# Performance work log

Measured on AMD Instinct MI355X. Metric: run time of the kernel, lower is better.

## Reference

```python
import jax, jax.numpy as jnp
import numpy as np

B, T, H, W = 4, 1024, 27, 48
LOOKUP = 101          # must be odd
OUT_DIM = 128
NBINS = 512           # 8 levels per RGB channel -> 8^3


def setup_inputs() -> dict:
    key = jax.random.key(0)
    k1, k2 = jax.random.split(key, 2)
    frames = jax.random.randint(k1, (B, T, H, W, 3), 0, 256, dtype=jnp.int32)
    # nn.Linear(lookup_window, output_dim): weight [out,in] in torch; store transposed [in,out]
    bound = 1.0 / np.sqrt(LOOKUP)
    fc_w = jax.random.uniform(k2, (LOOKUP, OUT_DIM), jnp.float32, -bound, bound)
    fc_b = jnp.zeros((OUT_DIM,), dtype=jnp.float32)
    return {"frames": frames, "fc_w": fc_w, "fc_b": fc_b}


def _color_histograms(frames):
    b, t, h, w, _ = frames.shape
    flat = frames.reshape(b * t, h * w, 3)
    # bit-pack RGB into 9-bit bin id: (R>>5)<<6 | (G>>5)<<3 | (B>>5)
    bins = ((flat[..., 0] >> 5) << 6) + ((flat[..., 1] >> 5) << 3) + (flat[..., 2] >> 5)
    bins = bins + (jnp.arange(b * t, dtype=jnp.int32) << 9)[:, None]  # per-frame offset
    hist = jax.ops.segment_sum(
        jnp.ones((b * t * h * w,), jnp.float32),
        bins.reshape(-1),
        num_segments=b * t * NBINS,
    ).reshape(b, t, NBINS)
    # F.normalize(p=2, dim=2): x / max(||x||, eps)
    norm = jnp.sqrt(jnp.sum(hist * hist, axis=2, keepdims=True))
    return hist / jnp.maximum(norm, 1e-12)


def reference(frames, fc_w, fc_b):
    x = _color_histograms(frames)             # [b, t, 512]
    b, t, _ = x.shape
    sims = jnp.einsum('bic,bjc->bij', x, x)   # [b, t, t]
    pad = (LOOKUP - 1) // 2
    sims_pad = jnp.pad(sims, ((0, 0), (0, 0), (pad, pad)))  # [b, t, t+L-1]
    # windowed gather: out[b,i,j] = sims_pad[b, i, i+j]
    row = jnp.arange(t)[:, None]                     # [t, 1]
    col = row + jnp.arange(LOOKUP)[None, :]          # [t, L]
    win = sims_pad[:, row, col]                      # [b, t, L]
    return jax.nn.relu(jnp.einsum('btl,lo->bto', win, fc_w) + fc_b)
```

## Files before the change

### kernel.cpp

```cpp
#include <hip/hip_runtime.h>
#include <math.h>

#define NB 4
#define NT 1024
#define NPIX 1296
#define NBINS 512
#define LOOKUP 101
#define PADW 50
#define ODIM 128
#define MT 16
#define NWIN 116
#define WPAD 104

typedef _Float16 v8h __attribute__((ext_vector_type(8)));
typedef float v4f __attribute__((ext_vector_type(4)));

__global__ __launch_bounds__(256) void hist_kernel(const int* __restrict__ frames,
                                                   unsigned short* __restrict__ X) {
    const int wv = threadIdx.x >> 6;
    const int lane = threadIdx.x & 63;
    const int frame = blockIdx.x * 4 + wv;

    __shared__ unsigned int hist[4][NBINS];
    unsigned int* h = hist[wv];

#pragma unroll
    for (int k = 0; k < NBINS / 64; ++k) h[lane + 64 * k] = 0u;

    const int4* f4 = (const int4*)(frames + (size_t)frame * NPIX * 3);
    for (int g = lane; g < NPIX / 4; g += 64) {
        int4 a = f4[g * 3 + 0];
        int4 b = f4[g * 3 + 1];
        int4 c = f4[g * 3 + 2];
        int v[12] = {a.x, a.y, a.z, a.w, b.x, b.y, b.z, b.w, c.x, c.y, c.z, c.w};
#pragma unroll
        for (int p = 0; p < 4; ++p) {
            int bin = ((v[3 * p] >> 5) << 6) | ((v[3 * p + 1] >> 5) << 3) | (v[3 * p + 2] >> 5);
            atomicAdd(&h[bin], 1u);
        }
    }

    float cnt[8];
    float local = 0.f;
#pragma unroll
    for (int k = 0; k < 8; ++k) {
        cnt[k] = (float)h[lane + 64 * k];
        local += cnt[k] * cnt[k];
    }
    for (int off = 32; off >= 1; off >>= 1) local += __shfl_xor(local, off, 64);
    float inv = 1.0f / fmaxf(sqrtf(local), 1e-12f);

    unsigned short* xr = X + (size_t)frame * NBINS;
#pragma unroll
    for (int k = 0; k < 8; ++k) {
        union { _Float16 h16; unsigned short u; } cv;
        cv.h16 = (_Float16)(cnt[k] * inv);
        xr[lane + 64 * k] = cv.u;
    }
}

__global__ __launch_bounds__(512) void simsfc_kernel(const unsigned short* __restrict__ Xu,
                                                     const float* __restrict__ w,
                                                     const float* __restrict__ bias,
                                                     float* __restrict__ out) {
    const int bid = blockIdx.x;
    const int tile = ((bid & 7) << 5) | (bid >> 3);
    const int b = tile >> 6;
    const int t0 = (tile & 63) * MT;
    const int tid = threadIdx.x;
    const int L = tid & 63;
    const int ntile = tid >> 6;

    const _Float16* Xh = (const _Float16*)Xu + (size_t)b * NT * NBINS;

    __shared__ float win_s[MT][WPAD];

    const _Float16* Ap = Xh + (size_t)(t0 + (L & 15)) * NBINS + 8 * (L >> 4);
    const int n = ntile * 16 + (L & 15);
    const int jl = t0 - PADW + n;
    const int jc = min(max(jl, 0), NT - 1);
    const _Float16* Bp = Xh + (size_t)jc * NBINS + 8 * (L >> 4);

    v4f acc = {0.f, 0.f, 0.f, 0.f};
#pragma unroll
    for (int s = 0; s < 16; ++s) {
        v8h a = *(const v8h*)(Ap + 32 * s);
        v8h bb = *(const v8h*)(Bp + 32 * s);
        acc = __builtin_amdgcn_mfma_f32_16x16x32_f16(a, bb, acc, 0, 0, 0);
    }

    const bool jvalid = (jl >= 0) && (jl < NT);
#pragma unroll
    for (int r = 0; r < 4; ++r) {
        const int m = 4 * (L >> 4) + r;
        const int l = n - m;
        if ((unsigned)l <= 100u) win_s[m][l] = jvalid ? acc[r] : 0.f;
    }
    __syncthreads();

    const int m = tid >> 5;
    const int ch = (tid & 31) * 4;
    v4f a4 = *(const v4f*)(bias + ch);
#pragma unroll 4
    for (int l = 0; l < LOOKUP; ++l) {
        float wl = win_s[m][l];
        v4f wv = *(const v4f*)(w + l * ODIM + ch);
        a4.x = fmaf(wl, wv.x, a4.x);
        a4.y = fmaf(wl, wv.y, a4.y);
        a4.z = fmaf(wl, wv.z, a4.z);
        a4.w = fmaf(wl, wv.w, a4.w);
    }
    a4.x = fmaxf(a4.x, 0.f); a4.y = fmaxf(a4.y, 0.f);
    a4.z = fmaxf(a4.z, 0.f); a4.w = fmaxf(a4.w, 0.f);
    *(v4f*)(out + (size_t)(b * NT + t0 + m) * ODIM + ch) = a4;
}

extern "C" void kernel_launch(void* const* d_in, const int* in_sizes, int n_in,
                              void* d_out, int out_size, void* d_ws, size_t ws_size,
                              hipStream_t stream) {
    const int*   frames = (const int*)d_in[0];
    const float* fc_w   = (const float*)d_in[1];
    const float* fc_b   = (const float*)d_in[2];
    float* out = (float*)d_out;

    unsigned short* X = (unsigned short*)d_ws;

    hist_kernel  <<<NB * NT / 4, 256, 0, stream>>>(frames, X);
    simsfc_kernel<<<NB * NT / MT, 512, 0, stream>>>(X, fc_w, fc_b, out);
}
```

Before: 114.4 us.

## Fuse histogram and similarity kernels via cooperative launch with grid sync

Merges the histogram kernel and the similarity+FC kernel into one cooperative kernel of 256 blocks × 512 threads. Each block first builds and normalizes histograms for 16 frames (two per wave), then a grid-wide sync is followed by the MFMA similarity and windowed FC stage. This removes a second kernel launch and the gap between the two launches. In exchange the histogram phase now runs on only 256 blocks instead of 1024, and the grid sync adds a barrier cost.

```diff
diff --git a/kernel.cpp b/kernel.cpp
--- a/kernel.cpp
+++ b/kernel.cpp
@@ -1,5 +1,8 @@
 #include <hip/hip_runtime.h>
+#include <hip/hip_cooperative_groups.h>
 #include <math.h>
+
+namespace cg = cooperative_groups;
 
 #define NB 4
 #define NT 1024
@@ -9,71 +12,89 @@
 #define PADW 50
 #define ODIM 128
 #define MT 16
-#define NWIN 116
 #define WPAD 104
+#define NBLK 256
+#define NTHR 512
 
 typedef _Float16 v8h __attribute__((ext_vector_type(8)));
 typedef float v4f __attribute__((ext_vector_type(4)));
 
-__global__ __launch_bounds__(256) void hist_kernel(const int* __restrict__ frames,
-                                                   unsigned short* __restrict__ X) {
-    const int wv = threadIdx.x >> 6;
-    const int lane = threadIdx.x & 63;
-    const int frame = blockIdx.x * 4 + wv;
-
-    __shared__ unsigned int hist[4][NBINS];
-    unsigned int* h = hist[wv];
-
-#pragma unroll
-    for (int k = 0; k < NBINS / 64; ++k) h[lane + 64 * k] = 0u;
-
-    const int4* f4 = (const int4*)(frames + (size_t)frame * NPIX * 3);
-    for (int g = lane; g < NPIX / 4; g += 64) {
-        int4 a = f4[g * 3 + 0];
-        int4 b = f4[g * 3 + 1];
-        int4 c = f4[g * 3 + 2];
-        int v[12] = {a.x, a.y, a.z, a.w, b.x, b.y, b.z, b.w, c.x, c.y, c.z, c.w};
-#pragma unroll
-        for (int p = 0; p < 4; ++p) {
-            int bin = ((v[3 * p] >> 5) << 6) | ((v[3 * p + 1] >> 5) << 3) | (v[3 * p + 2] >> 5);
-            atomicAdd(&h[bin], 1u);
-        }
-    }
-
-    float cnt[8];
-    float local = 0.f;
-#pragma unroll
-    for (int k = 0; k < 8; ++k) {
-        cnt[k] = (float)h[lane + 64 * k];
-        local += cnt[k] * cnt[k];
-    }
-    for (int off = 32; off >= 1; off >>= 1) local += __shfl_xor(local, off, 64);
-    float inv = 1.0f / fmaxf(sqrtf(local), 1e-12f);
-
-    unsigned short* xr = X + (size_t)frame * NBINS;
-#pragma unroll
-    for (int k = 0; k < 8; ++k) {
-        union { _Float16 h16; unsigned short u; } cv;
-        cv.h16 = (_Float16)(cnt[k] * inv);
-        xr[lane + 64 * k] = cv.u;
-    }
-}
-
-__global__ __launch_bounds__(512) void simsfc_kernel(const unsigned short* __restrict__ Xu,
+__global__ __launch_bounds__(NTHR) void fused_kernel(const int* __restrict__ frames,
+                                                     unsigned short* __restrict__ X,
                                                      const float* __restrict__ w,
                                                      const float* __restrict__ bias,
                                                      float* __restrict__ out) {
+    const int tid = threadIdx.x;
+    const int wv = tid >> 6;
+    const int lane = tid & 63;
     const int bid = blockIdx.x;
     const int tile = ((bid & 7) << 5) | (bid >> 3);
     const int b = tile >> 6;
     const int t0 = (tile & 63) * MT;
-    const int tid = threadIdx.x;
+
+    __shared__ unsigned int hist[8][NBINS];
+    __shared__ float win_s[MT][WPAD];
+
+    unsigned int* h = hist[wv];
+#pragma unroll
+    for (int rep = 0; rep < 2; ++rep) {
+        const int frame = 16 * tile + 2 * wv + rep;
+
+#pragma unroll
+        for (int k = 0; k < NBINS / 64; ++k) h[lane + 64 * k] = 0u;
+
+        const int4* f4 = (const int4*)(frames + (size_t)frame * NPIX * 3);
+#pragma unroll
+        for (int it = 0; it < 5; ++it) {
+            const int g = lane + 64 * it;
+            int4 a = f4[g * 3 + 0];
+            int4 bb = f4[g * 3 + 1];
+            int4 c = f4[g * 3 + 2];
+            int v[12] = {a.x, a.y, a.z, a.w, bb.x, bb.y, bb.z, bb.w, c.x, c.y, c.z, c.w};
+#pragma unroll
+            for (int p = 0; p < 4; ++p) {
+                int bin = ((v[3 * p] >> 5) << 6) | ((v[3 * p + 1] >> 5) << 3) | (v[3 * p + 2] >> 5);
+                atomicAdd(&h[bin], 1u);
+            }
+        }
+        if (lane < 4) {
+            const int g = 320 + lane;
+            int4 a = f4[g * 3 + 0];
+            int4 bb = f4[g * 3 + 1];
+            int4 c = f4[g * 3 + 2];
+            int v[12] = {a.x, a.y, a.z, a.w, bb.x, bb.y, bb.z, bb.w, c.x, c.y, c.z, c.w};
+#pragma unroll
+            for (int p = 0; p < 4; ++p) {
+                int bin = ((v[3 * p] >> 5) << 6) | ((v[3 * p + 1] >> 5) << 3) | (v[3 * p + 2] >> 5);
+                atomicAdd(&h[bin], 1u);
+            }
+        }
+
+        float cnt[8];
+        float local = 0.f;
+#pragma unroll
+        for (int k = 0; k < 8; ++k) {
+            cnt[k] = (float)h[lane + 64 * k];
+            local += cnt[k] * cnt[k];
+        }
+        for (int off = 32; off >= 1; off >>= 1) local += __shfl_xor(local, off, 64);
+        const float inv = 1.0f / fmaxf(sqrtf(local), 1e-12f);
+
+        unsigned short* xr = X + (size_t)frame * NBINS;
+#pragma unroll
+        for (int k = 0; k < 8; ++k) {
+            union { _Float16 h16; unsigned short u; } cv;
+            cv.h16 = (_Float16)(cnt[k] * inv);
+            xr[lane + 64 * k] = cv.u;
+        }
+    }
+
+    __threadfence();
+    cg::this_grid().sync();
+
+    const _Float16* Xh = (const _Float16*)X + (size_t)b * NT * NBINS;
     const int L = tid & 63;
     const int ntile = tid >> 6;
-
-    const _Float16* Xh = (const _Float16*)Xu + (size_t)b * NT * NBINS;
-
-    __shared__ float win_s[MT][WPAD];
 
     const _Float16* Ap = Xh + (size_t)(t0 + (L & 15)) * NBINS + 8 * (L >> 4);
     const int n = ntile * 16 + (L & 15);
@@ -104,11 +125,11 @@
 #pragma unroll 4
     for (int l = 0; l < LOOKUP; ++l) {
         float wl = win_s[m][l];
-        v4f wv = *(const v4f*)(w + l * ODIM + ch);
-        a4.x = fmaf(wl, wv.x, a4.x);
-        a4.y = fmaf(wl, wv.y, a4.y);
-        a4.z = fmaf(wl, wv.z, a4.z);
-        a4.w = fmaf(wl, wv.w, a4.w);
+        v4f wv4 = *(const v4f*)(w + l * ODIM + ch);
+        a4.x = fmaf(wl, wv4.x, a4.x);
+        a4.y = fmaf(wl, wv4.y, a4.y);
+        a4.z = fmaf(wl, wv4.z, a4.z);
+        a4.w = fmaf(wl, wv4.w, a4.w);
     }
     a4.x = fmaxf(a4.x, 0.f); a4.y = fmaxf(a4.y, 0.f);
     a4.z = fmaxf(a4.z, 0.f); a4.w = fmaxf(a4.w, 0.f);
@@ -125,6 +146,7 @@
 
     unsigned short* X = (unsigned short*)d_ws;
 
-    hist_kernel  <<<NB * NT / 4, 256, 0, stream>>>(frames, X);
-    simsfc_kernel<<<NB * NT / MT, 512, 0, stream>>>(X, fc_w, fc_b, out);
+    void* args[] = {(void*)&frames, (void*)&X, (void*)&fc_w, (void*)&fc_b, (void*)&out};
+    hipLaunchCooperativeKernel((void*)fused_kernel, dim3(NBLK), dim3(NTHR),
+                               args, 0, stream);
 }
```

New measurement: 220.9 us. +93.1%, slower.
